# Kernel optimization log

Hardware: AMD Instinct MI355X
Metric: run time of the kernel (lower is better)

Reference implementation:

```python
import jax, jax.numpy as jnp
import numpy as np
from jax import lax

B, S, T = 16, 256, 800
V, D, M, H = 256, 512, 80, 1024
NH = 4; HD = D // NH; EH = 256  # encoder LSTM hidden per direction


def setup_inputs() -> dict:
    key = jax.random.key(0)
    it = iter(jax.random.split(key, 40))
    def rn(shape, s=0.05):
        return jax.random.normal(next(it), shape, jnp.float32) * s
    return dict(
        text_inputs=jax.random.randint(next(it), (B, S), 0, V),
        mel_targets=jax.random.normal(next(it), (B, T, M), jnp.float32),
        emb=rn((V, D), 0.1),
        conv_w=rn((3, D, D, 5)), conv_b=rn((3, D)),
        bn_gamma=jnp.ones((3, D)), bn_beta=jnp.zeros((3, D)),
        bn_mean=rn((3, D)), bn_var=jnp.ones((3, D)),
        enc_Wih_f=rn((4 * EH, D)), enc_Whh_f=rn((4 * EH, EH)), enc_b_f=rn((4 * EH,)),
        enc_Wih_b=rn((4 * EH, D)), enc_Whh_b=rn((4 * EH, EH)), enc_b_b=rn((4 * EH,)),
        Wq=rn((D, M)), bq=rn((D,)), Wk=rn((D, D)), bk=rn((D,)),
        Wv=rn((D, D)), bv=rn((D,)), Wo=rn((D, D)), bo=rn((D,)),
        dec_Wih1=rn((4 * H, D + M)), dec_b1=rn((4 * H,)),
        dec_Wih2=rn((4 * H, H)), dec_b2=rn((4 * H,)),
        mel_W=rn((M, H)), mel_b=rn((M,)),
        stop_W=rn((1, H)), stop_b=rn((1,)),
    )


def _lstm_cell_zero(x, Wih, b):
    # single-step LSTM cell from zero (h, c); original resets state every timestep
    g = x @ Wih.T + b
    i, f, gg, o = jnp.split(g, 4, axis=-1)
    c = jax.nn.sigmoid(i) * jnp.tanh(gg)  # c0 = 0 -> forget gate contributes nothing
    return jax.nn.sigmoid(o) * jnp.tanh(c)


def _lstm_scan(xs, Wih, Whh, b, hdim, reverse):
    # xs: (S, B, in); PyTorch gate order i,f,g,o
    def step(carry, xt):
        h, c = carry
        g = xt @ Wih.T + h @ Whh.T + b
        i, f, gg, o = jnp.split(g, 4, axis=-1)
        c = jax.nn.sigmoid(f) * c + jax.nn.sigmoid(i) * jnp.tanh(gg)
        h = jax.nn.sigmoid(o) * jnp.tanh(c)
        return (h, c), h
    z = jnp.zeros((xs.shape[1], hdim), xs.dtype)
    _, hs = lax.scan(step, (z, z), xs, reverse=reverse)
    return hs


def reference(text_inputs, mel_targets, emb, conv_w, conv_b, bn_gamma, bn_beta, bn_mean, bn_var, enc_Wih_f, enc_Whh_f, enc_b_f, enc_Wih_b, enc_Whh_b, enc_b_b, Wq, bq, Wk, bk, Wv, bv, Wo, bo, dec_Wih1, dec_b1, dec_Wih2, dec_b2, mel_W, mel_b, stop_W, stop_b):
    b_, t_, m_ = mel_targets.shape
    # ---- encoder ----
    x = emb[text_inputs].transpose(0, 2, 1)  # (B, D, S)
    for i in range(conv_w.shape[0]):
        x = lax.conv_general_dilated(x, conv_w[i], (1,), [(2, 2)], dimension_numbers=('NCH', 'OIH', 'NCH')) + conv_b[i][None, :, None]
        x = bn_gamma[i][None, :, None] * (x - bn_mean[i][None, :, None]) * lax.rsqrt(bn_var[i][None, :, None] + 1e-5) + bn_beta[i][None, :, None]
        x = jax.nn.relu(x)  # dropout in eval mode -> identity
    xs = x.transpose(2, 0, 1)  # (S, B, D)
    hf = _lstm_scan(xs, enc_Wih_f, enc_Whh_f, enc_b_f, EH, False)
    hb = _lstm_scan(xs, enc_Wih_b, enc_Whh_b, enc_b_b, EH, True)
    enc = jnp.concatenate([hf, hb], -1).transpose(1, 0, 2)  # (B, S, D)
    # ---- decoder (teacher forcing): per-step query = previous mel frame ----
    dec_in = jnp.concatenate([jnp.zeros((b_, 1, m_), mel_targets.dtype), mel_targets[:, :-1]], axis=1)  # (B, T, M)
    q = (dec_in @ Wq.T + bq).reshape(b_, t_, NH, HD)
    k = (enc @ Wk.T + bk).reshape(b_, -1, NH, HD)
    v = (enc @ Wv.T + bv).reshape(b_, -1, NH, HD)
    scores = jnp.einsum('bqhd,bkhd->bhqk', q, k) * (1.0 / np.sqrt(HD)).astype(np.float32)
    attn = jax.nn.softmax(scores, axis=-1)
    ctx = jnp.einsum('bhqk,bkhd->bqhd', attn, v).reshape(b_, t_, D) @ Wo.T + bo
    xcat = jnp.concatenate([ctx, dec_in], axis=-1)  # (B, T, D+M)
    # original re-inits decoder LSTM state each timestep -> stateless per-step cells
    h1 = _lstm_cell_zero(xcat, dec_Wih1, dec_b1)
    h2 = _lstm_cell_zero(h1, dec_Wih2, dec_b2)
    mel = h2 @ mel_W.T + mel_b      # (B, T, 80)
    stop = h2 @ stop_W.T + stop_b   # (B, T, 1) - logits (no sigmoid in training path)
    return mel, stop
```

## Files before the change

kernel.cpp:

```cpp
#include <hip/hip_runtime.h>
#include <hip/hip_bf16.h>
#include <math.h>

#define B_ 16
#define S_ 256
#define T_ 800
#define V_ 256
#define D_ 512
#define M_ 80
#define H_ 1024
#define NH_ 4
#define HD_ 128
#define EH_ 256

using bf16x8 = __attribute__((ext_vector_type(8))) short;
using f32x4  = __attribute__((ext_vector_type(4))) float;
typedef _Float16 half8 __attribute__((ext_vector_type(8)));

__device__ __forceinline__ float sigf(float x) { return 1.f / (1.f + __expf(-x)); }
__device__ __forceinline__ float tanhfast(float x) {
    float e = __expf(2.f * x);
    return 1.f - 2.f / (e + 1.f);
}

__device__ __forceinline__ unsigned short f2bf(float f) {
    unsigned int u = __float_as_uint(f);
    unsigned int r = (u + 0x7FFFu + ((u >> 16) & 1u)) >> 16;
    return (unsigned short)r;
}
__device__ __forceinline__ float bf2f(unsigned short u) {
    return __uint_as_float(((unsigned int)u) << 16);
}
__device__ __forceinline__ unsigned short h2u(_Float16 x) {
    union { _Float16 f; unsigned short u; } c; c.f = x; return c.u;
}

__device__ __forceinline__ void gl_lds16(const unsigned short* g, unsigned short* l) {
    __builtin_amdgcn_global_load_lds((const __attribute__((address_space(1))) void*)g,
                                     (__attribute__((address_space(3))) void*)l, 16, 0, 0);
}

__global__ __launch_bounds__(256) void gemm_mfma(
    const unsigned short* __restrict__ A, const unsigned short* __restrict__ Bw,
    void* __restrict__ Cv, const float* __restrict__ bias,
    int M, int N, int K, int ldc, int epi,
    const float* __restrict__ cb, const float* __restrict__ gam,
    const float* __restrict__ bet, const float* __restrict__ mu,
    const float* __restrict__ va)
{
    __shared__ unsigned short As[4096];
    __shared__ unsigned short Bs[4096];
    const int tid = threadIdx.x, w = tid >> 6, lane = tid & 63;
    const int bm = blockIdx.y * 128, bn = blockIdx.x * 128;
    const int wr = w >> 1, wc = w & 1;

    f32x4 acc[4][4];
#pragma unroll
    for (int m = 0; m < 4; ++m)
#pragma unroll
        for (int n = 0; n < 4; ++n) acc[m][n] = (f32x4){0.f, 0.f, 0.f, 0.f};

    const int r0 = w * 16 + (lane >> 2);
    const int k8 = (lane & 3) * 8;
    const unsigned short* Ag = A + (size_t)(bm + r0) * K + k8;
    const unsigned short* Bg = Bw + (size_t)(bn + r0) * K + k8;
    unsigned short* Al = As + w * 512;
    unsigned short* Bl = Bs + w * 512;

    for (int k0 = 0; k0 < K; k0 += 32) {
        __syncthreads();
        gl_lds16(Ag + k0, Al);
        gl_lds16(Ag + (size_t)64 * K + k0, Al + 2048);
        gl_lds16(Bg + k0, Bl);
        gl_lds16(Bg + (size_t)64 * K + k0, Bl + 2048);
        __syncthreads();
        bf16x8 a[4], b[4];
#pragma unroll
        for (int m = 0; m < 4; ++m)
            a[m] = *(const bf16x8*)(As + (wr * 64 + m * 16 + (lane & 15)) * 32 + (lane >> 4) * 8);
#pragma unroll
        for (int n = 0; n < 4; ++n)
            b[n] = *(const bf16x8*)(Bs + (wc * 64 + n * 16 + (lane & 15)) * 32 + (lane >> 4) * 8);
#pragma unroll
        for (int m = 0; m < 4; ++m)
#pragma unroll
            for (int n = 0; n < 4; ++n)
                acc[m][n] = __builtin_amdgcn_mfma_f32_16x16x32_bf16(a[m], b[n], acc[m][n], 0, 0, 0);
    }

    const int cr = (lane >> 4) * 4, ccol = lane & 15;
#pragma unroll
    for (int m = 0; m < 4; ++m)
#pragma unroll
        for (int n = 0; n < 4; ++n) {
            const int col = bn + wc * 64 + n * 16 + ccol;
            const float bv = (bias && !(epi == 4 && col >= 80)) ? bias[col] : 0.f;
#pragma unroll
            for (int j = 0; j < 4; ++j) {
                const int row = bm + wr * 64 + m * 16 + cr + j;
                float v = acc[m][n][j] + bv;
                if (epi == 1) {
                    float x = v + cb[col];
                    v = fmaxf(0.f, gam[col] * (x - mu[col]) * rsqrtf(va[col] + 1e-5f) + bet[col]);
                }
                if (epi == 2) {
                    ((unsigned short*)Cv)[(size_t)row * ldc + col] = f2bf(v);
                } else if (epi == 3) {
                    const int bb2 = row >> 8, ss = row & 255, hh = col >> 7, dd = col & 127;
                    ((unsigned short*)Cv)[((size_t)(bb2 * 4 + hh) * 128 + dd) * 256 + ss] = f2bf(v);
                } else if (epi == 4) {
                    if (col < 80) ((float*)Cv)[(size_t)row * ldc + col] = v;
                } else {
                    ((float*)Cv)[(size_t)row * ldc + col] = v;
                }
            }
        }
}

__global__ __launch_bounds__(256) void attn_qksm(
    const unsigned short* __restrict__ q, const unsigned short* __restrict__ k,
    unsigned short* __restrict__ probs)
{
    __shared__ unsigned short As[2048];
    __shared__ unsigned short Bs[8192];
    __shared__ float redm[64][4];
    __shared__ float reds[64][4];
    const int tid = threadIdx.x, wid = tid >> 6, lane = tid & 63;
    const int l15 = lane & 15, bq = lane >> 4;
    const int bm = blockIdx.x * 64;
    const int z = blockIdx.y, b = z >> 2, h = z & 3;

    const unsigned short* A  = q + ((size_t)b * T_) * 512 + h * 128;
    const unsigned short* Bw = k + ((size_t)b * S_) * 512 + h * 128;

    f32x4 acc[4][4];
#pragma unroll
    for (int m = 0; m < 4; ++m)
#pragma unroll
        for (int n = 0; n < 4; ++n) acc[m][n] = (f32x4){0.f, 0.f, 0.f, 0.f};

    const int r0 = wid * 16 + (lane >> 2);
    const int k8 = (lane & 3) * 8;

    for (int k0 = 0; k0 < 128; k0 += 32) {
        __syncthreads();
        gl_lds16(A + (size_t)(bm + r0) * 512 + k0 + k8, As + wid * 512);
        gl_lds16(Bw + (size_t)r0 * 512 + k0 + k8,          Bs + wid * 512);
        gl_lds16(Bw + (size_t)(64 + r0) * 512 + k0 + k8,   Bs + 2048 + wid * 512);
        gl_lds16(Bw + (size_t)(128 + r0) * 512 + k0 + k8,  Bs + 4096 + wid * 512);
        gl_lds16(Bw + (size_t)(192 + r0) * 512 + k0 + k8,  Bs + 6144 + wid * 512);
        __syncthreads();
        bf16x8 a[4], bb[4];
#pragma unroll
        for (int m = 0; m < 4; ++m)
            a[m] = *(const bf16x8*)(As + (m * 16 + l15) * 32 + bq * 8);
#pragma unroll
        for (int n = 0; n < 4; ++n)
            bb[n] = *(const bf16x8*)(Bs + (wid * 64 + n * 16 + l15) * 32 + bq * 8);
#pragma unroll
        for (int m = 0; m < 4; ++m)
#pragma unroll
            for (int n = 0; n < 4; ++n)
                acc[m][n] = __builtin_amdgcn_mfma_f32_16x16x32_bf16(a[m], bb[n], acc[m][n], 0, 0, 0);
    }

    const int cr = (lane >> 4) * 4, ccol = lane & 15;
    const float SC = 0.08838834764831843f;

    float lmax[4][4];
#pragma unroll
    for (int m = 0; m < 4; ++m)
#pragma unroll
        for (int j = 0; j < 4; ++j) {
            float v = fmaxf(fmaxf(acc[m][0][j], acc[m][1][j]),
                            fmaxf(acc[m][2][j], acc[m][3][j]));
#pragma unroll
            for (int off = 1; off < 16; off <<= 1) v = fmaxf(v, __shfl_xor(v, off));
            lmax[m][j] = v;
            if (ccol == 0) redm[m * 16 + cr + j][wid] = v;
        }
    __syncthreads();
    float lsum[4][4];
#pragma unroll
    for (int m = 0; m < 4; ++m)
#pragma unroll
        for (int j = 0; j < 4; ++j) {
            const int r = m * 16 + cr + j;
            float mx = fmaxf(fmaxf(redm[r][0], redm[r][1]), fmaxf(redm[r][2], redm[r][3]));
            lmax[m][j] = mx;
            float s = 0.f;
#pragma unroll
            for (int n = 0; n < 4; ++n) {
                float p = __expf((acc[m][n][j] - mx) * SC);
                acc[m][n][j] = p;
                s += p;
            }
#pragma unroll
            for (int off = 1; off < 16; off <<= 1) s += __shfl_xor(s, off);
            lsum[m][j] = s;
            if (ccol == 0) reds[r][wid] = s;
        }
    __syncthreads();
#pragma unroll
    for (int m = 0; m < 4; ++m)
#pragma unroll
        for (int j = 0; j < 4; ++j) {
            const int r = m * 16 + cr + j;
            const int row = bm + r;
            if (row >= T_) continue;
            const float inv = 1.f / (reds[r][0] + reds[r][1] + reds[r][2] + reds[r][3]);
#pragma unroll
            for (int n = 0; n < 4; ++n)
                probs[((size_t)z * T_ + row) * 256 + wid * 64 + n * 16 + ccol] =
                    f2bf(acc[m][n][j] * inv);
        }
}

__global__ __launch_bounds__(256) void attn_pv(
    const unsigned short* __restrict__ probs, const unsigned short* __restrict__ vT,
    unsigned short* __restrict__ ctx)
{
    __shared__ unsigned short As[4096];
    __shared__ unsigned short Bs[4096];
    const int tid = threadIdx.x, w = tid >> 6, lane = tid & 63;
    const int bm = blockIdx.y * 128;
    const int z = blockIdx.z, b = z >> 2, h = z & 3;
    const int wr = w >> 1, wc = w & 1;

    const unsigned short* A  = probs + (size_t)z * T_ * 256;
    const unsigned short* Bw = vT + (size_t)z * 128 * 256;

    f32x4 acc[4][4];
#pragma unroll
    for (int m = 0; m < 4; ++m)
#pragma unroll
        for (int n = 0; n < 4; ++n) acc[m][n] = (f32x4){0.f, 0.f, 0.f, 0.f};

    const int r0 = w * 16 + (lane >> 2);
    const int k8 = (lane & 3) * 8;
    const unsigned short* Ag = A + (size_t)(bm + r0) * 256 + k8;
    const unsigned short* Bg = Bw + (size_t)r0 * 256 + k8;
    unsigned short* Al = As + w * 512;
    unsigned short* Bl = Bs + w * 512;

    for (int k0 = 0; k0 < 256; k0 += 32) {
        __syncthreads();
        gl_lds16(Ag + k0, Al);
        gl_lds16(Ag + (size_t)64 * 256 + k0, Al + 2048);
        gl_lds16(Bg + k0, Bl);
        gl_lds16(Bg + (size_t)64 * 256 + k0, Bl + 2048);
        __syncthreads();
        bf16x8 a[4], bfr[4];
#pragma unroll
        for (int m = 0; m < 4; ++m)
            a[m] = *(const bf16x8*)(As + (wr * 64 + m * 16 + (lane & 15)) * 32 + (lane >> 4) * 8);
#pragma unroll
        for (int n = 0; n < 4; ++n)
            bfr[n] = *(const bf16x8*)(Bs + (wc * 64 + n * 16 + (lane & 15)) * 32 + (lane >> 4) * 8);
#pragma unroll
        for (int m = 0; m < 4; ++m)
#pragma unroll
            for (int n = 0; n < 4; ++n)
                acc[m][n] = __builtin_amdgcn_mfma_f32_16x16x32_bf16(a[m], bfr[n], acc[m][n], 0, 0, 0);
    }

    const int cr = (lane >> 4) * 4, ccol = lane & 15;
#pragma unroll
    for (int m = 0; m < 4; ++m)
#pragma unroll
        for (int n = 0; n < 4; ++n) {
            const int col = wc * 64 + n * 16 + ccol;
#pragma unroll
            for (int j = 0; j < 4; ++j) {
                const int row = bm + wr * 64 + m * 16 + cr + j;
                if (row < T_)
                    ctx[((size_t)b * T_ + row) * 512 + h * 128 + col] = f2bf(acc[m][n][j]);
            }
        }
}

__global__ void im2col_bf(const float* __restrict__ in, unsigned short* __restrict__ out)
{
    int idx = blockIdx.x * 256 + threadIdx.x;
    if (idx >= B_ * S_ * 2560) return;
    int r = idx / 2560, cc = idx % 2560;
    int din = cc / 5, kk = cc % 5;
    int b = r >> 8, s = r & 255;
    int sp = s + kk - 2;
    float v = (sp >= 0 && sp < S_) ? in[((size_t)b * S_ + sp) * D_ + din] : 0.f;
    out[idx] = f2bf(v);
}

__global__ void transp_bf(const float* __restrict__ in, unsigned short* __restrict__ out)
{
    int idx = blockIdx.x * 256 + threadIdx.x;
    if (idx >= B_ * S_ * D_) return;
    int d = idx & 511;
    int sb = idx >> 9;
    int s = sb >> 4, b = sb & 15;
    out[idx] = f2bf(in[((size_t)b * S_ + s) * D_ + d]);
}

__global__ void hist2enc(const _Float16* __restrict__ hist, unsigned short* __restrict__ enc)
{
    int idx = blockIdx.x * 256 + threadIdx.x;
    if (idx >= B_ * S_ * D_) return;
    int d = idx & 511;
    int bs = idx >> 9;
    int b = bs >> 8, s = bs & 255;
    int dir = d >> 8, hid = d & 255;
    enc[idx] = f2bf((float)hist[(((size_t)(dir * 16 + b) * 256 + s) * 256) + hid]);
}

__global__ void cvt_all(
    const float* __restrict__ conv_w, const float* __restrict__ Wih_f,
    const float* __restrict__ Wih_b, const float* __restrict__ Wk,
    const float* __restrict__ Wv, const float* __restrict__ Wq,
    const float* __restrict__ Wo, const float* __restrict__ Wih1,
    const float* __restrict__ Wih2, const float* __restrict__ melW,
    const int* __restrict__ txt, const float* __restrict__ emb,
    const float* __restrict__ mel,
    unsigned short* __restrict__ cWc, unsigned short* __restrict__ cWif,
    unsigned short* __restrict__ cWib, unsigned short* __restrict__ cWk,
    unsigned short* __restrict__ cWv, unsigned short* __restrict__ cWq,
    unsigned short* __restrict__ cWo, unsigned short* __restrict__ cW1,
    unsigned short* __restrict__ cW2, unsigned short* __restrict__ cWm,
    float* __restrict__ xs, unsigned short* __restrict__ din,
    unsigned short* __restrict__ xcat)
{
    int idx = blockIdx.x * 256 + threadIdx.x;
    if (idx < 3932160) { cWc[idx] = f2bf(conv_w[idx]); return; }
    idx -= 3932160;
    if (idx < 524288) { cWif[idx] = f2bf(Wih_f[idx]); return; }
    idx -= 524288;
    if (idx < 524288) { cWib[idx] = f2bf(Wih_b[idx]); return; }
    idx -= 524288;
    if (idx < 262144) { cWk[idx] = f2bf(Wk[idx]); return; }
    idx -= 262144;
    if (idx < 262144) { cWv[idx] = f2bf(Wv[idx]); return; }
    idx -= 262144;
    if (idx < 49152) {
        int r = idx / 96, k = idx - r * 96;
        cWq[idx] = (k < 80) ? f2bf(Wq[(size_t)r * 80 + k]) : 0;
        return;
    }
    idx -= 49152;
    if (idx < 262144) { cWo[idx] = f2bf(Wo[idx]); return; }
    idx -= 262144;
    if (idx < 1867776) {
        int n = idx / 608, k = idx - n * 608;
        int orig = (n < 1024) ? n : n + 1024;
        cW1[idx] = (k < 592) ? f2bf(Wih1[(size_t)orig * 592 + k]) : 0;
        return;
    }
    idx -= 1867776;
    if (idx < 3145728) {
        int n = idx >> 10, k = idx & 1023;
        int orig = (n < 1024) ? n : n + 1024;
        cW2[idx] = f2bf(Wih2[(size_t)orig * 1024 + k]);
        return;
    }
    idx -= 3145728;
    if (idx < 131072) {
        int r = idx >> 10, k = idx & 1023;
        cWm[idx] = (r < 80) ? f2bf(melW[(size_t)r * 1024 + k]) : 0;
        return;
    }
    idx -= 131072;
    if (idx < B_ * S_ * D_) {
        int bs = idx >> 9, dd = idx & 511;
        xs[idx] = emb[(size_t)txt[bs] * D_ + dd];
        return;
    }
    idx -= B_ * S_ * D_;
    if (idx < B_ * T_ * 96) {
        int r = idx / 96, j = idx - r * 96;
        int b = r / T_, t = r - b * T_;
        float v = (j < M_ && t > 0) ? mel[((size_t)b * T_ + t - 1) * M_ + j] : 0.f;
        unsigned short bv = f2bf(v);
        din[(size_t)r * 96 + j] = bv;
        xcat[(size_t)r * 608 + 512 + j] = bv;
        return;
    }
}

__global__ void dec_cellb2(const unsigned short* __restrict__ g, const float* __restrict__ b,
                           unsigned short* __restrict__ h, int rows)
{
    int idx = blockIdx.x * 256 + threadIdx.x;
    if (idx >= rows * 512) return;
    int r = idx >> 9, j2 = (idx & 511) * 2;
    const unsigned short* gr = g + (size_t)r * 3072;
    ushort2 vi = *(const ushort2*)(gr + j2);
    ushort2 vg = *(const ushort2*)(gr + 1024 + j2);
    ushort2 vo = *(const ushort2*)(gr + 2048 + j2);
    float i0 = sigf(bf2f(vi.x) + b[j2]),          i1 = sigf(bf2f(vi.y) + b[j2 + 1]);
    float g0 = tanhfast(bf2f(vg.x) + b[2048 + j2]), g1 = tanhfast(bf2f(vg.y) + b[2048 + j2 + 1]);
    float o0 = sigf(bf2f(vo.x) + b[3072 + j2]),   o1 = sigf(bf2f(vo.y) + b[3072 + j2 + 1]);
    ushort2 o;
    o.x = f2bf(o0 * tanhfast(i0 * g0));
    o.y = f2bf(o1 * tanhfast(i1 * g1));
    *(ushort2*)(h + (size_t)r * 1024 + j2) = o;
}

__global__ __launch_bounds__(256) void stop_head(
    const unsigned short* __restrict__ h2, const float* __restrict__ sw,
    const float* __restrict__ sb, float* __restrict__ out)
{
    int row = blockIdx.x * 4 + (threadIdx.x >> 6);
    int lane = threadIdx.x & 63;
    const unsigned short* hr = h2 + (size_t)row * H_;
    float acc = 0.f;
#pragma unroll
    for (int i = 0; i < H_; i += 64) acc += bf2f(hr[i + lane]) * sw[i + lane];
    for (int off = 32; off; off >>= 1) acc += __shfl_xor(acc, off);
    if (lane == 0) out[row] = acc + sb[0];
}

__global__ __launch_bounds__(1024, 4) void lstm_persist9(
    const float* __restrict__ gi_f, const float* __restrict__ gi_b,
    const float* __restrict__ Wf, const float* __restrict__ Wb,
    _Float16* __restrict__ hist,
    unsigned long long* __restrict__ hstage)
{
    const int blk = blockIdx.x;
    const int dir = blk >> 1, half = blk & 1;
    const float* gi = dir ? gi_b : gi_f;
    const float* W  = dir ? Wb : Wf;
    const int tid = threadIdx.x, wid = tid >> 6, lane = tid & 63;
    const int l15 = lane & 15, q = lane >> 4;
    const int half4 = half * 4, ph4 = (half ^ 1) * 4;

    __shared__ _Float16 h_lds[16][264];
    __shared__ float exch[512][17];

    half8 wOA[4], wPA[4], wOB[4], wPB[4];
    {
        const int gt0 = wid >> 3, hb0 = wid & 7;
        const int gt1 = (wid + 16) >> 3;
        const float* wr0 = W + (size_t)(gt0 * 256 + half * 128 + hb0 * 16 + l15) * 256;
        const float* wr1 = W + (size_t)(gt1 * 256 + half * 128 + hb0 * 16 + l15) * 256;
#pragma unroll
        for (int i = 0; i < 4; ++i) {
            const int kO = (half4 + i) * 32 + q * 8;
            const int kP = (ph4 + i) * 32 + q * 8;
            half8 a, b, c, d;
#pragma unroll
            for (int j = 0; j < 8; ++j) {
                a[j] = (_Float16)wr0[kO + j];
                b[j] = (_Float16)wr0[kP + j];
                c[j] = (_Float16)wr1[kO + j];
                d[j] = (_Float16)wr1[kP + j];
            }
            wOA[i] = a; wPA[i] = b; wOB[i] = c; wPB[i] = d;
        }
    }
    for (int i = tid; i < 16 * 264; i += 1024) ((_Float16*)h_lds)[i] = (_Float16)0.f;
    for (int i = tid; i < 512 * 17; i += 1024) ((float*)exch)[i] = 0.f;

    const int hid = tid & 127;
    const int ba  = tid >> 7;
    const int bb  = ba + 8;
    const int gh  = half * 128 + hid;
    const int pc  = (half ^ 1) * 128 + hid;
    float c0 = 0.f, c1 = 0.f;

    const int exr0 = (wid >> 3) * 128 + (wid & 7) * 16 + l15;
    const int exr1 = ((wid + 16) >> 3) * 128 + (wid & 7) * 16 + l15;

    const int own_base = ((dir * 2 + half) * 8 + ba) * 128 + hid;
    const int par_base = ((dir * 2 + (half ^ 1)) * 8 + ba) * 128 + hid;

    float gp0[4], gp1[4];
    {
        const int s0 = dir ? 255 : 0;
        const float* g0 = gi + ((size_t)s0 * 16 + ba) * 1024 + gh;
        const float* g1 = gi + ((size_t)s0 * 16 + bb) * 1024 + gh;
#pragma unroll
        for (int g2 = 0; g2 < 4; ++g2) { gp0[g2] = g0[g2 * 256]; gp1[g2] = g1[g2 * 256]; }
    }
    __syncthreads();

    for (int step = 0; step < 256; ++step) {
        const int s = dir ? (255 - step) : step;
        const unsigned int tag = (unsigned int)(step + 1);
        const int slot = (step & 1) * 4096;

        float h0, h1;
        {
            float xi = exch[hid][ba] + gp0[0];
            float xf = exch[128 + hid][ba] + gp0[1];
            float xg = exch[256 + hid][ba] + gp0[2];
            float xo = exch[384 + hid][ba] + gp0[3];
            float ig = sigf(xi), fg = sigf(xf), gg = tanhfast(xg), og = sigf(xo);
            c0 = fg * c0 + ig * gg; h0 = og * tanhfast(c0);
            xi = exch[hid][bb] + gp1[0];
            xf = exch[128 + hid][bb] + gp1[1];
            xg = exch[256 + hid][bb] + gp1[2];
            xo = exch[384 + hid][bb] + gp1[3];
            ig = sigf(xi); fg = sigf(xf); gg = tanhfast(xg); og = sigf(xo);
            c1 = fg * c1 + ig * gg; h1 = og * tanhfast(c1);
        }
        {
            unsigned int d32 = (unsigned int)h2u((_Float16)h0) |
                               ((unsigned int)h2u((_Float16)h1) << 16);
            unsigned long long wv = ((unsigned long long)tag << 32) | d32;
            __hip_atomic_store(&hstage[slot + own_base], wv,
                               __ATOMIC_RELAXED, __HIP_MEMORY_SCOPE_AGENT);
        }
        h_lds[ba][gh] = (_Float16)h0;
        h_lds[bb][gh] = (_Float16)h1;
        hist[(((size_t)(dir * 16 + ba) * 256 + s) * 256) + gh] = (_Float16)h0;
        hist[(((size_t)(dir * 16 + bb) * 256 + s) * 256) + gh] = (_Float16)h1;
        if (step < 255) {
            const int s2 = dir ? (254 - step) : (step + 1);
            const float* g0 = gi + ((size_t)s2 * 16 + ba) * 1024 + gh;
            const float* g1 = gi + ((size_t)s2 * 16 + bb) * 1024 + gh;
#pragma unroll
            for (int g2 = 0; g2 < 4; ++g2) { gp0[g2] = g0[g2 * 256]; gp1[g2] = g1[g2 * 256]; }
        }
        __syncthreads();

        if (step < 255) {
            f32x4 acc0 = (f32x4){0.f, 0.f, 0.f, 0.f};
            f32x4 acc1 = (f32x4){0.f, 0.f, 0.f, 0.f};
            const _Float16* hrow = &h_lds[l15][0];
#pragma unroll
            for (int i = 0; i < 4; ++i) {
                half8 a = *(const half8*)(hrow + (half4 + i) * 32 + q * 8);
                acc0 = __builtin_amdgcn_mfma_f32_16x16x32_f16(a, wOA[i], acc0, 0, 0, 0);
                acc1 = __builtin_amdgcn_mfma_f32_16x16x32_f16(a, wOB[i], acc1, 0, 0, 0);
            }
            {
                unsigned long long pv;
                do {
                    pv = __hip_atomic_load(&hstage[slot + par_base],
                                           __ATOMIC_RELAXED, __HIP_MEMORY_SCOPE_AGENT);
                } while ((unsigned int)(pv >> 32) != tag);
                unsigned int d32 = (unsigned int)pv;
                *(unsigned short*)&h_lds[ba][pc] = (unsigned short)(d32 & 0xFFFF);
                *(unsigned short*)&h_lds[bb][pc] = (unsigned short)(d32 >> 16);
            }
            __syncthreads();
#pragma unroll
            for (int i = 0; i < 4; ++i) {
                half8 a = *(const half8*)(hrow + (ph4 + i) * 32 + q * 8);
                acc0 = __builtin_amdgcn_mfma_f32_16x16x32_f16(a, wPA[i], acc0, 0, 0, 0);
                acc1 = __builtin_amdgcn_mfma_f32_16x16x32_f16(a, wPB[i], acc1, 0, 0, 0);
            }
            *(f32x4*)&exch[exr0][q * 4] = acc0;
            *(f32x4*)&exch[exr1][q * 4] = acc1;
            __syncthreads();
        }
    }
}

static inline void launch_mfma(hipStream_t st, const unsigned short* A, const unsigned short* B,
                               void* C, const float* bias, int M, int N, int K, int ldc, int epi = 0,
                               const float* cb = nullptr, const float* gam = nullptr,
                               const float* bet = nullptr, const float* mu = nullptr,
                               const float* va = nullptr)
{
    dim3 grid(N / 128, M / 128);
    gemm_mfma<<<grid, 256, 0, st>>>(A, B, C, bias, M, N, K, ldc, epi, cb, gam, bet, mu, va);
}

extern "C" void kernel_launch(void* const* d_in, const int* in_sizes, int n_in,
                              void* d_out, int out_size, void* d_ws, size_t ws_size,
                              hipStream_t stream)
{
    const int*   text   = (const int*)d_in[0];
    const float* mel_t  = (const float*)d_in[1];
    const float* emb    = (const float*)d_in[2];
    const float* conv_w = (const float*)d_in[3];
    const float* conv_b = (const float*)d_in[4];
    const float* bn_g   = (const float*)d_in[5];
    const float* bn_b   = (const float*)d_in[6];
    const float* bn_m   = (const float*)d_in[7];
    const float* bn_v   = (const float*)d_in[8];
    const float* Wih_f  = (const float*)d_in[9];
    const float* Whh_f  = (const float*)d_in[10];
    const float* b_f    = (const float*)d_in[11];
    const float* Wih_b  = (const float*)d_in[12];
    const float* Whh_b  = (const float*)d_in[13];
    const float* b_b    = (const float*)d_in[14];
    const float* Wq     = (const float*)d_in[15];
    const float* bq     = (const float*)d_in[16];
    const float* Wk     = (const float*)d_in[17];
    const float* bk     = (const float*)d_in[18];
    const float* Wv     = (const float*)d_in[19];
    const float* bv     = (const float*)d_in[20];
    const float* Wo     = (const float*)d_in[21];
    const float* bo     = (const float*)d_in[22];
    const float* Wih1   = (const float*)d_in[23];
    const float* b1     = (const float*)d_in[24];
    const float* Wih2   = (const float*)d_in[25];
    const float* b2     = (const float*)d_in[26];
    const float* melW   = (const float*)d_in[27];
    const float* melb   = (const float*)d_in[28];
    const float* stopW  = (const float*)d_in[29];
    const float* stopb  = (const float*)d_in[30];
    float* out = (float*)d_out;
    (void)in_sizes; (void)n_in; (void)out_size; (void)ws_size;

    float* ws = (float*)d_ws;
    float* big  = ws;
    float* pool = ws + 13107200;

    unsigned long long* hstage = (unsigned long long*)(ws + 6000000);

    float*          gi_f   = pool + 0;
    float*          gi_b   = pool + 4194304;
    unsigned short* enc_bf = (unsigned short*)(pool + 8388608);
    float*          P0     = pool + 9437184;
    float*          P1     = pool + 11534336;
    unsigned short* xsT    = (unsigned short*)(pool + 13631488);
    _Float16*       hist   = (_Float16*)(pool + 14155776);
    unsigned short* kbf    = (unsigned short*)(pool + 0);
    unsigned short* vT     = (unsigned short*)(pool + 1048576);
    unsigned short* qbf    = (unsigned short*)(pool + 2097152);
    unsigned short* probs  = (unsigned short*)(pool + 9437184);
    unsigned short* dinb   = (unsigned short*)(pool + 16008192);
    unsigned short* ctxb   = (unsigned short*)(pool + 16622592);
    unsigned short* gatesb = (unsigned short*)(pool + 0);
    unsigned short* h2b    = (unsigned short*)big;
    unsigned short* h1b    = (unsigned short*)(big + 4000000);
    unsigned short* xcat   = (unsigned short*)(pool + 19899392);
    float*          WB     = pool + 23790592;
    unsigned short* cWc  = (unsigned short*)(WB + 0);
    unsigned short* cWif = (unsigned short*)(WB + 1966080);
    unsigned short* cWib = (unsigned short*)(WB + 2228224);
    unsigned short* cWk  = (unsigned short*)(WB + 2490368);
    unsigned short* cWv  = (unsigned short*)(WB + 2621440);
    unsigned short* cWq  = (unsigned short*)(WB + 2752512);
    unsigned short* cWo  = (unsigned short*)(WB + 2777088);
    unsigned short* cW1  = (unsigned short*)(WB + 2908160);
    unsigned short* cW2  = (unsigned short*)(WB + 3842048);
    unsigned short* cWm  = (unsigned short*)(WB + 5414912);

    auto ceil256 = [](int n) { return (n + 255) / 256; };

    hipMemsetAsync(hstage, 0, 8192 * 8, stream);

    cvt_all<<<ceil256(10960896 + B_ * S_ * D_ + B_ * T_ * 96), 256, 0, stream>>>(
        conv_w, Wih_f, Wih_b, Wk, Wv, Wq, Wo, Wih1, Wih2, melW,
        text, emb, mel_t,
        cWc, cWif, cWib, cWk, cWv, cWq, cWo, cW1, cW2, cWm,
        P0, dinb, xcat);

    float* cin = P0;
    float* cout = P1;
    for (int l = 0; l < 3; ++l) {
        im2col_bf<<<ceil256(B_ * S_ * 2560), 256, 0, stream>>>(cin, (unsigned short*)big);
        launch_mfma(stream, (unsigned short*)big, cWc + (size_t)l * 512 * 2560,
                    cout, nullptr, B_ * S_, 512, 2560, 512, 1,
                    conv_b + l * 512, bn_g + l * 512, bn_b + l * 512, bn_m + l * 512, bn_v + l * 512);
        float* tmp = cin; cin = cout; cout = tmp;
    }
    transp_bf<<<ceil256(B_ * S_ * D_), 256, 0, stream>>>(cin, xsT);

    launch_mfma(stream, xsT, cWif, gi_f, b_f, S_ * B_, 1024, 512, 1024);
    launch_mfma(stream, xsT, cWib, gi_b, b_b, S_ * B_, 1024, 512, 1024);
    lstm_persist9<<<4, 1024, 0, stream>>>(gi_f, gi_b, Whh_f, Whh_b, hist, hstage);
    hist2enc<<<ceil256(B_ * S_ * D_), 256, 0, stream>>>(hist, enc_bf);

    launch_mfma(stream, enc_bf, cWk, kbf, bk, B_ * S_, 512, 512, 512, 2);
    launch_mfma(stream, enc_bf, cWv, vT, bv, B_ * S_, 512, 512, 0, 3);
    launch_mfma(stream, dinb, cWq, qbf, bq, B_ * T_, 512, 96, 512, 2);

    attn_qksm<<<dim3(13, 64), 256, 0, stream>>>(qbf, kbf, probs);
    attn_pv<<<dim3(1, 7, 64), 256, 0, stream>>>(probs, vT, ctxb);

    launch_mfma(stream, ctxb, cWo, xcat, bo, B_ * T_, 512, 512, 608, 2);

    launch_mfma(stream, xcat, cW1, gatesb, nullptr, B_ * T_, 3072, 608, 3072, 2);
    dec_cellb2<<<ceil256(B_ * T_ * 512), 256, 0, stream>>>(gatesb, b1, h1b, B_ * T_);
    launch_mfma(stream, h1b, cW2, gatesb, nullptr, B_ * T_, 3072, 1024, 3072, 2);
    dec_cellb2<<<ceil256(B_ * T_ * 512), 256, 0, stream>>>(gatesb, b2, h2b, B_ * T_);

    launch_mfma(stream, h2b, cWm, out, melb, B_ * T_, 128, 1024, 80, 4);
    stop_head<<<(B_ * T_) / 4, 256, 0, stream>>>(h2b, stopW, stopb, out + (size_t)B_ * T_ * M_);
}
```

Before: 1.585 ms.

## Fuse im2col into conv GEMM, merge K/V projections and stop head, drop transposes

The conv layers now use an implicit-GEMM kernel that gathers shifted bf16 input rows directly, with a zero buffer for padding. This removes the im2col materialization and the fp32 intermediates, and the weights are reordered to a kk-major layout to match. The encoder LSTM input GEMMs read the conv output through a row permutation, which replaces the transpose kernel. The K and V projections are merged into one N=1024 GEMM, and the stop head is folded into the mel GEMM as an extra output column, cutting several launches and memory passes.

```diff
diff --git a/kernel.cpp b/kernel.cpp
--- a/kernel.cpp
+++ b/kernel.cpp
@@ -43,10 +43,8 @@
 __global__ __launch_bounds__(256) void gemm_mfma(
     const unsigned short* __restrict__ A, const unsigned short* __restrict__ Bw,
     void* __restrict__ Cv, const float* __restrict__ bias,
-    int M, int N, int K, int ldc, int epi,
-    const float* __restrict__ cb, const float* __restrict__ gam,
-    const float* __restrict__ bet, const float* __restrict__ mu,
-    const float* __restrict__ va)
+    int M, int N, int K, int ldc, int epi, int aperm,
+    const float* __restrict__ cb)
 {
     __shared__ unsigned short As[4096];
     __shared__ unsigned short Bs[4096];
@@ -62,15 +60,21 @@
 
     const int r0 = w * 16 + (lane >> 2);
     const int k8 = (lane & 3) * 8;
-    const unsigned short* Ag = A + (size_t)(bm + r0) * K + k8;
+    int ar0 = bm + r0, ar1 = bm + r0 + 64;
+    if (aperm) {
+        ar0 = ((ar0 & 15) << 8) | (ar0 >> 4);
+        ar1 = ((ar1 & 15) << 8) | (ar1 >> 4);
+    }
+    const unsigned short* Ag0 = A + (size_t)ar0 * K + k8;
+    const unsigned short* Ag1 = A + (size_t)ar1 * K + k8;
     const unsigned short* Bg = Bw + (size_t)(bn + r0) * K + k8;
     unsigned short* Al = As + w * 512;
     unsigned short* Bl = Bs + w * 512;
 
     for (int k0 = 0; k0 < K; k0 += 32) {
         __syncthreads();
-        gl_lds16(Ag + k0, Al);
-        gl_lds16(Ag + (size_t)64 * K + k0, Al + 2048);
+        gl_lds16(Ag0 + k0, Al);
+        gl_lds16(Ag1 + k0, Al + 2048);
         gl_lds16(Bg + k0, Bl);
         gl_lds16(Bg + (size_t)64 * K + k0, Bl + 2048);
         __syncthreads();
@@ -94,25 +98,106 @@
 #pragma unroll
         for (int n = 0; n < 4; ++n) {
             const int col = bn + wc * 64 + n * 16 + ccol;
-            const float bv = (bias && !(epi == 4 && col >= 80)) ? bias[col] : 0.f;
+            float bv;
+            if (epi == 5)      bv = (col < 512) ? bias[col] : cb[col - 512];
+            else if (epi == 4) bv = (col < 80) ? bias[col] : (col == 80 ? cb[0] : 0.f);
+            else               bv = bias ? bias[col] : 0.f;
 #pragma unroll
             for (int j = 0; j < 4; ++j) {
                 const int row = bm + wr * 64 + m * 16 + cr + j;
                 float v = acc[m][n][j] + bv;
-                if (epi == 1) {
-                    float x = v + cb[col];
-                    v = fmaxf(0.f, gam[col] * (x - mu[col]) * rsqrtf(va[col] + 1e-5f) + bet[col]);
-                }
                 if (epi == 2) {
                     ((unsigned short*)Cv)[(size_t)row * ldc + col] = f2bf(v);
-                } else if (epi == 3) {
-                    const int bb2 = row >> 8, ss = row & 255, hh = col >> 7, dd = col & 127;
-                    ((unsigned short*)Cv)[((size_t)(bb2 * 4 + hh) * 128 + dd) * 256 + ss] = f2bf(v);
+                } else if (epi == 5) {
+                    if (col < 512) {
+                        ((unsigned short*)Cv)[(size_t)row * 512 + col] = f2bf(v);
+                    } else {
+                        unsigned short* vTo = (unsigned short*)Cv + 2097152;
+                        const int c2 = col - 512, hh = c2 >> 7, dd = c2 & 127;
+                        const int bb2 = row >> 8, ss = row & 255;
+                        vTo[((size_t)(bb2 * 4 + hh) * 128 + dd) * 256 + ss] = f2bf(v);
+                    }
                 } else if (epi == 4) {
-                    if (col < 80) ((float*)Cv)[(size_t)row * ldc + col] = v;
+                    if (col < 80)       ((float*)Cv)[(size_t)row * ldc + col] = v;
+                    else if (col == 80) ((float*)Cv)[1024000 + row] = v;
                 } else {
                     ((float*)Cv)[(size_t)row * ldc + col] = v;
                 }
+            }
+        }
+}
+
+__global__ __launch_bounds__(256) void conv_mfma(
+    const unsigned short* __restrict__ xin, const unsigned short* __restrict__ Bw,
+    unsigned short* __restrict__ xout,
+    const float* __restrict__ cb, const float* __restrict__ gam,
+    const float* __restrict__ bet, const float* __restrict__ mu,
+    const float* __restrict__ va, const unsigned short* __restrict__ zbuf)
+{
+    __shared__ unsigned short As[4096];
+    __shared__ unsigned short Bs[4096];
+    const int tid = threadIdx.x, w = tid >> 6, lane = tid & 63;
+    const int bm = blockIdx.y * 128, bn = blockIdx.x * 128;
+    const int wr = w >> 1, wc = w & 1;
+
+    f32x4 acc[4][4];
+#pragma unroll
+    for (int m = 0; m < 4; ++m)
+#pragma unroll
+        for (int n = 0; n < 4; ++n) acc[m][n] = (f32x4){0.f, 0.f, 0.f, 0.f};
+
+    const int r0 = w * 16 + (lane >> 2);
+    const int k8 = (lane & 3) * 8;
+    const int gr0 = bm + r0, gr1 = bm + r0 + 64;
+    const int b0 = gr0 >> 8, s0 = gr0 & 255;
+    const int b1 = gr1 >> 8, s1 = gr1 & 255;
+    const unsigned short* Bg = Bw + (size_t)(bn + r0) * 2560 + k8;
+    unsigned short* Al = As + w * 512;
+    unsigned short* Bl = Bs + w * 512;
+
+    for (int k0 = 0; k0 < 2560; k0 += 32) {
+        const int kk = k0 >> 9;
+        const int d0 = k0 & 511;
+        const int s2a = s0 + kk - 2;
+        const int s2b = s1 + kk - 2;
+        const unsigned short* pa = (s2a >= 0 && s2a < 256)
+            ? xin + ((size_t)(b0 * 256 + s2a) * 512 + d0 + k8) : zbuf;
+        const unsigned short* pb = (s2b >= 0 && s2b < 256)
+            ? xin + ((size_t)(b1 * 256 + s2b) * 512 + d0 + k8) : zbuf;
+        __syncthreads();
+        gl_lds16(pa, Al);
+        gl_lds16(pb, Al + 2048);
+        gl_lds16(Bg + k0, Bl);
+        gl_lds16(Bg + (size_t)64 * 2560 + k0, Bl + 2048);
+        __syncthreads();
+        bf16x8 a[4], b[4];
+#pragma unroll
+        for (int m = 0; m < 4; ++m)
+            a[m] = *(const bf16x8*)(As + (wr * 64 + m * 16 + (lane & 15)) * 32 + (lane >> 4) * 8);
+#pragma unroll
+        for (int n = 0; n < 4; ++n)
+            b[n] = *(const bf16x8*)(Bs + (wc * 64 + n * 16 + (lane & 15)) * 32 + (lane >> 4) * 8);
+#pragma unroll
+        for (int m = 0; m < 4; ++m)
+#pragma unroll
+            for (int n = 0; n < 4; ++n)
+                acc[m][n] = __builtin_amdgcn_mfma_f32_16x16x32_bf16(a[m], b[n], acc[m][n], 0, 0, 0);
+    }
+
+    const int cr = (lane >> 4) * 4, ccol = lane & 15;
+#pragma unroll
+    for (int m = 0; m < 4; ++m)
+#pragma unroll
+        for (int n = 0; n < 4; ++n) {
+            const int col = bn + wc * 64 + n * 16 + ccol;
+            const float bc = cb[col], gm = gam[col], bt = bet[col];
+            const float mv = mu[col], iv = rsqrtf(va[col] + 1e-5f);
+#pragma unroll
+            for (int j = 0; j < 4; ++j) {
+                const int row = bm + wr * 64 + m * 16 + cr + j;
+                float x = acc[m][n][j] + bc;
+                float y = fmaxf(0.f, gm * (x - mv) * iv + bt);
+                xout[(size_t)row * 512 + col] = f2bf(y);
             }
         }
 }
@@ -167,7 +252,6 @@
     const int cr = (lane >> 4) * 4, ccol = lane & 15;
     const float SC = 0.08838834764831843f;
 
-    float lmax[4][4];
 #pragma unroll
     for (int m = 0; m < 4; ++m)
 #pragma unroll
@@ -176,18 +260,15 @@
                             fmaxf(acc[m][2][j], acc[m][3][j]));
 #pragma unroll
             for (int off = 1; off < 16; off <<= 1) v = fmaxf(v, __shfl_xor(v, off));
-            lmax[m][j] = v;
             if (ccol == 0) redm[m * 16 + cr + j][wid] = v;
         }
     __syncthreads();
-    float lsum[4][4];
 #pragma unroll
     for (int m = 0; m < 4; ++m)
 #pragma unroll
         for (int j = 0; j < 4; ++j) {
             const int r = m * 16 + cr + j;
             float mx = fmaxf(fmaxf(redm[r][0], redm[r][1]), fmaxf(redm[r][2], redm[r][3]));
-            lmax[m][j] = mx;
             float s = 0.f;
 #pragma unroll
             for (int n = 0; n < 4; ++n) {
@@ -197,7 +278,6 @@
             }
 #pragma unroll
             for (int off = 1; off < 16; off <<= 1) s += __shfl_xor(s, off);
-            lsum[m][j] = s;
             if (ccol == 0) reds[r][wid] = s;
         }
     __syncthreads();
@@ -277,28 +357,6 @@
                     ctx[((size_t)b * T_ + row) * 512 + h * 128 + col] = f2bf(acc[m][n][j]);
             }
         }
-}
-
-__global__ void im2col_bf(const float* __restrict__ in, unsigned short* __restrict__ out)
-{
-    int idx = blockIdx.x * 256 + threadIdx.x;
-    if (idx >= B_ * S_ * 2560) return;
-    int r = idx / 2560, cc = idx % 2560;
-    int din = cc / 5, kk = cc % 5;
-    int b = r >> 8, s = r & 255;
-    int sp = s + kk - 2;
-    float v = (sp >= 0 && sp < S_) ? in[((size_t)b * S_ + sp) * D_ + din] : 0.f;
-    out[idx] = f2bf(v);
-}
-
-__global__ void transp_bf(const float* __restrict__ in, unsigned short* __restrict__ out)
-{
-    int idx = blockIdx.x * 256 + threadIdx.x;
-    if (idx >= B_ * S_ * D_) return;
-    int d = idx & 511;
-    int sb = idx >> 9;
-    int s = sb >> 4, b = sb & 15;
-    out[idx] = f2bf(in[((size_t)b * S_ + s) * D_ + d]);
 }
 
 __global__ void hist2enc(const _Float16* __restrict__ hist, unsigned short* __restrict__ enc)
@@ -318,27 +376,36 @@
     const float* __restrict__ Wv, const float* __restrict__ Wq,
     const float* __restrict__ Wo, const float* __restrict__ Wih1,
     const float* __restrict__ Wih2, const float* __restrict__ melW,
+    const float* __restrict__ stopW,
     const int* __restrict__ txt, const float* __restrict__ emb,
     const float* __restrict__ mel,
     unsigned short* __restrict__ cWc, unsigned short* __restrict__ cWif,
-    unsigned short* __restrict__ cWib, unsigned short* __restrict__ cWk,
-    unsigned short* __restrict__ cWv, unsigned short* __restrict__ cWq,
-    unsigned short* __restrict__ cWo, unsigned short* __restrict__ cW1,
-    unsigned short* __restrict__ cW2, unsigned short* __restrict__ cWm,
-    float* __restrict__ xs, unsigned short* __restrict__ din,
+    unsigned short* __restrict__ cWib, unsigned short* __restrict__ cWkv,
+    unsigned short* __restrict__ cWq, unsigned short* __restrict__ cWo,
+    unsigned short* __restrict__ cW1, unsigned short* __restrict__ cW2,
+    unsigned short* __restrict__ cWm,
+    unsigned short* __restrict__ xb0, unsigned short* __restrict__ din,
     unsigned short* __restrict__ xcat)
 {
     int idx = blockIdx.x * 256 + threadIdx.x;
-    if (idx < 3932160) { cWc[idx] = f2bf(conv_w[idx]); return; }
+    if (idx < 3932160) {
+        int n = idx / 2560, c = idx - n * 2560;
+        int kk = c >> 9, din2 = c & 511;
+        cWc[idx] = f2bf(conv_w[(size_t)n * 2560 + din2 * 5 + kk]);
+        return;
+    }
     idx -= 3932160;
     if (idx < 524288) { cWif[idx] = f2bf(Wih_f[idx]); return; }
     idx -= 524288;
     if (idx < 524288) { cWib[idx] = f2bf(Wih_b[idx]); return; }
     idx -= 524288;
-    if (idx < 262144) { cWk[idx] = f2bf(Wk[idx]); return; }
-    idx -= 262144;
-    if (idx < 262144) { cWv[idx] = f2bf(Wv[idx]); return; }
-    idx -= 262144;
+    if (idx < 524288) {
+        int r = idx >> 9, k = idx & 511;
+        cWkv[idx] = (r < 512) ? f2bf(Wk[(size_t)r * 512 + k])
+                              : f2bf(Wv[(size_t)(r - 512) * 512 + k]);
+        return;
+    }
+    idx -= 524288;
     if (idx < 49152) {
         int r = idx / 96, k = idx - r * 96;
         cWq[idx] = (k < 80) ? f2bf(Wq[(size_t)r * 80 + k]) : 0;
@@ -363,13 +430,14 @@
     idx -= 3145728;
     if (idx < 131072) {
         int r = idx >> 10, k = idx & 1023;
-        cWm[idx] = (r < 80) ? f2bf(melW[(size_t)r * 1024 + k]) : 0;
+        cWm[idx] = (r < 80) ? f2bf(melW[(size_t)r * 1024 + k])
+                            : (r == 80 ? f2bf(stopW[k]) : 0);
         return;
     }
     idx -= 131072;
     if (idx < B_ * S_ * D_) {
         int bs = idx >> 9, dd = idx & 511;
-        xs[idx] = emb[(size_t)txt[bs] * D_ + dd];
+        xb0[idx] = f2bf(emb[(size_t)txt[bs] * D_ + dd]);
         return;
     }
     idx -= B_ * S_ * D_;
@@ -401,20 +469,6 @@
     o.x = f2bf(o0 * tanhfast(i0 * g0));
     o.y = f2bf(o1 * tanhfast(i1 * g1));
     *(ushort2*)(h + (size_t)r * 1024 + j2) = o;
-}
-
-__global__ __launch_bounds__(256) void stop_head(
-    const unsigned short* __restrict__ h2, const float* __restrict__ sw,
-    const float* __restrict__ sb, float* __restrict__ out)
-{
-    int row = blockIdx.x * 4 + (threadIdx.x >> 6);
-    int lane = threadIdx.x & 63;
-    const unsigned short* hr = h2 + (size_t)row * H_;
-    float acc = 0.f;
-#pragma unroll
-    for (int i = 0; i < H_; i += 64) acc += bf2f(hr[i + lane]) * sw[i + lane];
-    for (int off = 32; off; off >>= 1) acc += __shfl_xor(acc, off);
-    if (lane == 0) out[row] = acc + sb[0];
 }
 
 __global__ __launch_bounds__(1024, 4) void lstm_persist9(
@@ -556,13 +610,11 @@
 }
 
 static inline void launch_mfma(hipStream_t st, const unsigned short* A, const unsigned short* B,
-                               void* C, const float* bias, int M, int N, int K, int ldc, int epi = 0,
-                               const float* cb = nullptr, const float* gam = nullptr,
-                               const float* bet = nullptr, const float* mu = nullptr,
-                               const float* va = nullptr)
+                               void* C, const float* bias, int M, int N, int K, int ldc,
+                               int epi = 0, int aperm = 0, const float* cb = nullptr)
 {
     dim3 grid(N / 128, M / 128);
-    gemm_mfma<<<grid, 256, 0, st>>>(A, B, C, bias, M, N, K, ldc, epi, cb, gam, bet, mu, va);
+    gemm_mfma<<<grid, 256, 0, st>>>(A, B, C, bias, M, N, K, ldc, epi, aperm, cb);
 }
 
 extern "C" void kernel_launch(void* const* d_in, const int* in_sizes, int n_in,
@@ -608,13 +660,15 @@
     float* pool = ws + 13107200;
 
     unsigned long long* hstage = (unsigned long long*)(ws + 6000000);
+    const unsigned short* zbuf = (const unsigned short*)(hstage + 8192);
 
     float*          gi_f   = pool + 0;
     float*          gi_b   = pool + 4194304;
     unsigned short* enc_bf = (unsigned short*)(pool + 8388608);
-    float*          P0     = pool + 9437184;
-    float*          P1     = pool + 11534336;
-    unsigned short* xsT    = (unsigned short*)(pool + 13631488);
+    unsigned short* xb0    = (unsigned short*)(pool + 9437184);
+    unsigned short* xb1    = (unsigned short*)(pool + 10485760);
+    unsigned short* xb2    = (unsigned short*)(pool + 11534336);
+    unsigned short* xb3    = (unsigned short*)(pool + 12582912);
     _Float16*       hist   = (_Float16*)(pool + 14155776);
     unsigned short* kbf    = (unsigned short*)(pool + 0);
     unsigned short* vT     = (unsigned short*)(pool + 1048576);
@@ -630,8 +684,7 @@
     unsigned short* cWc  = (unsigned short*)(WB + 0);
     unsigned short* cWif = (unsigned short*)(WB + 1966080);
     unsigned short* cWib = (unsigned short*)(WB + 2228224);
-    unsigned short* cWk  = (unsigned short*)(WB + 2490368);
-    unsigned short* cWv  = (unsigned short*)(WB + 2621440);
+    unsigned short* cWkv = (unsigned short*)(WB + 2490368);
     unsigned short* cWq  = (unsigned short*)(WB + 2752512);
     unsigned short* cWo  = (unsigned short*)(WB + 2777088);
     unsigned short* cW1  = (unsigned short*)(WB + 2908160);
@@ -640,32 +693,30 @@
 
     auto ceil256 = [](int n) { return (n + 255) / 256; };
 
-    hipMemsetAsync(hstage, 0, 8192 * 8, stream);
+    hipMemsetAsync(hstage, 0, 8192 * 8 + 128, stream);
 
     cvt_all<<<ceil256(10960896 + B_ * S_ * D_ + B_ * T_ * 96), 256, 0, stream>>>(
-        conv_w, Wih_f, Wih_b, Wk, Wv, Wq, Wo, Wih1, Wih2, melW,
+        conv_w, Wih_f, Wih_b, Wk, Wv, Wq, Wo, Wih1, Wih2, melW, stopW,
         text, emb, mel_t,
-        cWc, cWif, cWib, cWk, cWv, cWq, cWo, cW1, cW2, cWm,
-        P0, dinb, xcat);
-
-    float* cin = P0;
-    float* cout = P1;
-    for (int l = 0; l < 3; ++l) {
-        im2col_bf<<<ceil256(B_ * S_ * 2560), 256, 0, stream>>>(cin, (unsigned short*)big);
-        launch_mfma(stream, (unsigned short*)big, cWc + (size_t)l * 512 * 2560,
-                    cout, nullptr, B_ * S_, 512, 2560, 512, 1,
-                    conv_b + l * 512, bn_g + l * 512, bn_b + l * 512, bn_m + l * 512, bn_v + l * 512);
-        float* tmp = cin; cin = cout; cout = tmp;
-    }
-    transp_bf<<<ceil256(B_ * S_ * D_), 256, 0, stream>>>(cin, xsT);
-
-    launch_mfma(stream, xsT, cWif, gi_f, b_f, S_ * B_, 1024, 512, 1024);
-    launch_mfma(stream, xsT, cWib, gi_b, b_b, S_ * B_, 1024, 512, 1024);
+        cWc, cWif, cWib, cWkv, cWq, cWo, cW1, cW2, cWm,
+        xb0, dinb, xcat);
+
+    {
+        dim3 grid(4, 32);
+        conv_mfma<<<grid, 256, 0, stream>>>(xb0, cWc,               xb1,
+            conv_b, bn_g, bn_b, bn_m, bn_v, zbuf);
+        conv_mfma<<<grid, 256, 0, stream>>>(xb1, cWc + 1310720,     xb2,
+            conv_b + 512, bn_g + 512, bn_b + 512, bn_m + 512, bn_v + 512, zbuf);
+        conv_mfma<<<grid, 256, 0, stream>>>(xb2, cWc + 2621440,     xb3,
+            conv_b + 1024, bn_g + 1024, bn_b + 1024, bn_m + 1024, bn_v + 1024, zbuf);
+    }
+
+    launch_mfma(stream, xb3, cWif, gi_f, b_f, S_ * B_, 1024, 512, 1024, 0, 1);
+    launch_mfma(stream, xb3, cWib, gi_b, b_b, S_ * B_, 1024, 512, 1024, 0, 1);
     lstm_persist9<<<4, 1024, 0, stream>>>(gi_f, gi_b, Whh_f, Whh_b, hist, hstage);
     hist2enc<<<ceil256(B_ * S_ * D_), 256, 0, stream>>>(hist, enc_bf);
 
-    launch_mfma(stream, enc_bf, cWk, kbf, bk, B_ * S_, 512, 512, 512, 2);
-    launch_mfma(stream, enc_bf, cWv, vT, bv, B_ * S_, 512, 512, 0, 3);
+    launch_mfma(stream, enc_bf, cWkv, kbf, bk, B_ * S_, 1024, 512, 512, 5, 0, bv);
     launch_mfma(stream, dinb, cWq, qbf, bq, B_ * T_, 512, 96, 512, 2);
 
     attn_qksm<<<dim3(13, 64), 256, 0, stream>>>(qbf, kbf, probs);
@@ -678,6 +729,5 @@
     launch_mfma(stream, h1b, cW2, gatesb, nullptr, B_ * T_, 3072, 1024, 3072, 2);
     dec_cellb2<<<ceil256(B_ * T_ * 512), 256, 0, stream>>>(gatesb, b2, h2b, B_ * T_);
 
-    launch_mfma(stream, h2b, cWm, out, melb, B_ * T_, 128, 1024, 80, 4);
-    stop_head<<<(B_ * T_) / 4, 256, 0, stream>>>(h2b, stopW, stopb, out + (size_t)B_ * T_ * M_);
-}
+    launch_mfma(stream, h2b, cWm, out, melb, B_ * T_, 128, 1024, 80, 4, 0, stopb);
+}
```

New measurement: 1.333 ms. 15.9% less time.
